# Kernel tuning notes

Measured on AMD Instinct MI355X. Metric: run time of the kernel, lower is better.

The kernel has to match this reference:

```python
import jax, jax.numpy as jnp
import numpy as np

B, N, D = 1, 128, 64
H, DH = 8, 64            # heads, per-head dim; dim_inner = dim*dim_head = 512
DI = H * DH              # 512
L = 2                    # max_degree
S = 1 + 2 * L            # 5 degree slots: (h, r_1..L, x_1..L)
MLP = 1024               # int(2.0 * dim_inner)
EPS = 1e-5


def _ln(x, g):
    m = x.mean(-1, keepdims=True)
    v = ((x - m) ** 2).mean(-1, keepdims=True)
    return (x - m) * jax.lax.rsqrt(v + EPS) * g


def setup_inputs() -> dict:
    key = jax.random.key(0)
    ks = jax.random.split(key, 16)
    rn = lambda k, s, sc=1.0: jax.random.normal(k, s, dtype=jnp.float32) * sc
    return {
        "h": rn(ks[0], (B, N, D)),
        "t_ij": rn(ks[1], (B, N, N, D)),
        "r1": rn(ks[2], (B, N, N, 3)),
        "r2": rn(ks[3], (B, N, N, 5)),
        "x1": rn(ks[4], (B, N, D, 3)),
        "x2": rn(ks[5], (B, N, D, 5)),
        "g_hi": jnp.ones((D,), jnp.float32),
        "g_hj": jnp.ones((D,), jnp.float32),
        "Wq": rn(ks[6], (D, DI), D ** -0.5),
        "Wk": rn(ks[7], (D, DI), D ** -0.5),
        "Wv1": rn(ks[8], (D, MLP), D ** -0.5),
        "bv1": jnp.zeros((MLP,), jnp.float32),
        "Wv2": rn(ks[9], (MLP, S * DI), MLP ** -0.5),
        "bv2": jnp.zeros((S * DI,), jnp.float32),
        "Wp1": rn(ks[10], (D, MLP), D ** -0.5),
        "bp1": jnp.zeros((MLP,), jnp.float32),
        "Wp2": rn(ks[11], (MLP, S * DI), MLP ** -0.5),
        "bp2": jnp.zeros((S * DI,), jnp.float32),
        "Wev": rn(ks[12], (D, S * DI), D ** -0.5),
        "Wc": rn(ks[13], (DI, D), DI ** -0.5),
    }


def reference(h, t_ij, r1, r2, x1, x2, g_hi, g_hj, Wq, Wk, Wv1, bv1, Wv2, bv2,
              Wp1, bp1, Wp2, bp2, Wev, Wc):
    b, n, d = h.shape
    hi, hj = _ln(h, g_hi), _ln(h, g_hj)
    q = (hi @ Wq).reshape(b, n, H, DH).transpose(0, 2, 1, 3)                # b h i d
    k = (hj @ Wk).reshape(b, n, H, DH).transpose(0, 2, 1, 3)                # b h j d
    vals = (jax.nn.silu(hj @ Wv1 + bv1) @ Wv2 + bv2)
    vals = vals.reshape(b, n, S, H, DH).transpose(0, 3, 1, 2, 4)            # b h j s d
    pav = (jax.nn.silu(hj @ Wp1 + bp1) @ Wp2 + bp2)
    pav = pav.reshape(b, n, S, H, DH).transpose(0, 3, 1, 2, 4)              # b h j s d
    # NOTE: source uses to_edge_values for BOTH edge keys and edge values (to_edge_keys is dead code)
    ev = (t_ij @ Wev).reshape(b, n, n, S, H, DH).transpose(0, 4, 1, 2, 3, 5)  # b h i j s d
    sim_num = jnp.einsum('bhid,bhjd->bhij', q, k)                           # b h i j
    sim_den = jnp.einsum('bhid,bhijsd->bhis', q, ev)                        # b h i s
    attn = sim_num[..., None] / sim_den[:, :, :, None, :]                   # b h i j s (quotient attention)
    sea = attn[..., None] * vals[:, :, None] + ev * pav[:, :, None]         # b h i j s d
    out = sea.transpose(0, 2, 3, 4, 1, 5).reshape(b, n, n, S, DI) @ Wc      # b i j s D
    # split sizes (1, L, L) along the s axis: h scale, r_ij scales, x scales
    h_new = h + out[:, :, :, 0, :].sum(axis=2)                              # sum over neighbors j
    xs, rs = (x1, x2), (r1, r2)
    x_new = [jnp.einsum('bjdm,bijd->bidm', xs[l], out[:, :, :, 1 + L + l, :])
             + jnp.einsum('bijm,bijd->bidm', rs[l], out[:, :, :, 1 + l, :])
             for l in range(L)]
    return (h_new, x_new[0], x_new[1])
```

## Files before the change

kernel.cpp:

```cpp
#include <hip/hip_runtime.h>
#include <hip/hip_bf16.h>

typedef __hip_bfloat16 bf16;
typedef __attribute__((ext_vector_type(8))) short short8;
typedef __attribute__((ext_vector_type(4))) float f32x4;

#define NN 128
#define DD_ 64
#define HH_ 8
#define DH_ 64
#define DI_ 512
#define SS_ 5
#define MLPD 1024
#define SDI 2560
#define KS2 4
#define KCM 64

__device__ __forceinline__ float wave_sum64(float v) {
#pragma unroll
    for (int off = 32; off > 0; off >>= 1) v += __shfl_xor(v, off, 64);
    return v;
}

__device__ __forceinline__ unsigned short f2bf_u(float f) {
    unsigned u = __float_as_uint(f);
    u += 0x7FFF + ((u >> 16) & 1);
    return (unsigned short)(u >> 16);
}
__device__ __forceinline__ float bfu2f(unsigned short s) {
    return __uint_as_float(((unsigned)s) << 16);
}
__device__ __forceinline__ unsigned pk2(unsigned short a, unsigned short b) {
    return (unsigned)a | ((unsigned)b << 16);
}

__global__ __launch_bounds__(256) void k_front(
    const float* __restrict__ h, const float* __restrict__ ghi, const float* __restrict__ ghj,
    const float* __restrict__ Wq, const float* __restrict__ Wk,
    const float* __restrict__ Wv1, const float* __restrict__ bv1,
    const float* __restrict__ Wp1, const float* __restrict__ bp1,
    float* __restrict__ q, float* __restrict__ k,
    float* __restrict__ a1, float* __restrict__ p1) {
    int i = blockIdx.x, ch = blockIdx.y, t = threadIdx.x;
    int d = t & 63;
    __shared__ float hib[DD_], hjb[DD_];
    float x = h[i * DD_ + d];
    float s = wave_sum64(x);
    float s2 = wave_sum64(x * x);
    float m = s * (1.0f / DD_);
    float v = s2 * (1.0f / DD_) - m * m;
    float r = rsqrtf(v + 1e-5f);
    float xc = (x - m) * r;
    if (t < 64) { hib[d] = xc * ghi[d]; hjb[d] = xc * ghj[d]; }
    __syncthreads();
    {
        int c = ch * 128 + (t & 127);
        const float* W = (t < 128) ? Wq : Wk;
        const float* hb = (t < 128) ? hib : hjb;
        float a = 0.f;
#pragma unroll 8
        for (int dd = 0; dd < DD_; dd++) a += hb[dd] * W[dd * DI_ + c];
        float* dstqk = (t < 128) ? q : k;
        dstqk[i * DI_ + c] = a;
    }
    {
        int c = ch * 256 + t;
        float av = 0.f, ap = 0.f;
#pragma unroll 4
        for (int dd = 0; dd < DD_; dd++) {
            float hv = hjb[dd];
            av += hv * Wv1[dd * MLPD + c];
            ap += hv * Wp1[dd * MLPD + c];
        }
        float xv = av + bv1[c], xp = ap + bp1[c];
        a1[i * MLPD + c] = xv / (1.0f + expf(-xv));
        p1[i * MLPD + c] = xp / (1.0f + expf(-xp));
    }
}

__global__ __launch_bounds__(256) void k_mid(
    const float* __restrict__ a1, const float* __restrict__ p1,
    const float* __restrict__ Wv2, const float* __restrict__ Wp2,
    float* __restrict__ part,
    const float* __restrict__ tij, const float* __restrict__ Wev,
    const float* __restrict__ q, float* __restrict__ rsd,
    const float* __restrict__ k, float* __restrict__ sn) {
    __shared__ __align__(16) unsigned char smem[30720];
    int b = blockIdx.x, t = threadIdx.x;
    if (b < 320) {
        unsigned short (*Ahi)[40] = (unsigned short (*)[40])(smem);
        unsigned short (*Alo)[40] = (unsigned short (*)[40])(smem + 10240);
        unsigned short (*Bhi)[40] = (unsigned short (*)[40])(smem + 20480);
        unsigned short (*Blo)[40] = (unsigned short (*)[40])(smem + 25600);
        int ct = b % 80, ks = b / 80;
        int c0 = ct * 64;
        bool isp = c0 >= 2560;
        int c0l = c0 - (isp ? 2560 : 0);
        const float* __restrict__ src = isp ? p1 : a1;
        const float* __restrict__ W = isp ? Wp2 : Wv2;
        int kbase = ks * 256;
        int lane = t & 63, wv = t >> 6;
        int l15 = lane & 15, quad = lane >> 4;
        f32x4 acc[2][4];
#pragma unroll
        for (int mt = 0; mt < 2; mt++)
#pragma unroll
            for (int nt = 0; nt < 4; nt++) acc[mt][nt] = (f32x4){0.f, 0.f, 0.f, 0.f};
        int aj = t >> 1, ak = (t & 1) * 16;
        int bc = t & 63, bk = (t >> 6) * 8;
        for (int kc = 0; kc < 8; kc++) {
            int k0 = kbase + kc * 32;
            __syncthreads();
            {
                unsigned short h16[16], l16[16];
                const float* ap = &src[(size_t)aj * MLPD + k0 + ak];
#pragma unroll
                for (int e = 0; e < 16; e += 4) {
                    float4 v = *(const float4*)(ap + e);
                    float vv[4] = {v.x, v.y, v.z, v.w};
#pragma unroll
                    for (int z = 0; z < 4; z++) {
                        unsigned short hb = f2bf_u(vv[z]);
                        h16[e + z] = hb;
                        l16[e + z] = f2bf_u(vv[z] - bfu2f(hb));
                    }
                }
                *(uint4*)&Ahi[aj][ak] = make_uint4(pk2(h16[0], h16[1]), pk2(h16[2], h16[3]),
                                                   pk2(h16[4], h16[5]), pk2(h16[6], h16[7]));
                *(uint4*)&Ahi[aj][ak + 8] = make_uint4(pk2(h16[8], h16[9]), pk2(h16[10], h16[11]),
                                                       pk2(h16[12], h16[13]), pk2(h16[14], h16[15]));
                *(uint4*)&Alo[aj][ak] = make_uint4(pk2(l16[0], l16[1]), pk2(l16[2], l16[3]),
                                                   pk2(l16[4], l16[5]), pk2(l16[6], l16[7]));
                *(uint4*)&Alo[aj][ak + 8] = make_uint4(pk2(l16[8], l16[9]), pk2(l16[10], l16[11]),
                                                       pk2(l16[12], l16[13]), pk2(l16[14], l16[15]));
            }
            {
                unsigned short h8[8], l8[8];
#pragma unroll
                for (int e = 0; e < 8; e++) {
                    float v = W[(size_t)(k0 + bk + e) * SDI + c0l + bc];
                    unsigned short hb = f2bf_u(v);
                    h8[e] = hb;
                    l8[e] = f2bf_u(v - bfu2f(hb));
                }
                *(uint4*)&Bhi[bc][bk] = make_uint4(pk2(h8[0], h8[1]), pk2(h8[2], h8[3]),
                                                   pk2(h8[4], h8[5]), pk2(h8[6], h8[7]));
                *(uint4*)&Blo[bc][bk] = make_uint4(pk2(l8[0], l8[1]), pk2(l8[2], l8[3]),
                                                   pk2(l8[4], l8[5]), pk2(l8[6], l8[7]));
            }
            __syncthreads();
            int ko = quad * 8;
            short8 a_h0 = *(const short8*)&Ahi[(wv * 2 + 0) * 16 + l15][ko];
            short8 a_l0 = *(const short8*)&Alo[(wv * 2 + 0) * 16 + l15][ko];
            short8 a_h1 = *(const short8*)&Ahi[(wv * 2 + 1) * 16 + l15][ko];
            short8 a_l1 = *(const short8*)&Alo[(wv * 2 + 1) * 16 + l15][ko];
#pragma unroll
            for (int nt = 0; nt < 4; nt++) {
                short8 b_h = *(const short8*)&Bhi[nt * 16 + l15][ko];
                short8 b_l = *(const short8*)&Blo[nt * 16 + l15][ko];
                acc[0][nt] = __builtin_amdgcn_mfma_f32_16x16x32_bf16(a_h0, b_h, acc[0][nt], 0, 0, 0);
                acc[0][nt] = __builtin_amdgcn_mfma_f32_16x16x32_bf16(a_h0, b_l, acc[0][nt], 0, 0, 0);
                acc[0][nt] = __builtin_amdgcn_mfma_f32_16x16x32_bf16(a_l0, b_h, acc[0][nt], 0, 0, 0);
                acc[1][nt] = __builtin_amdgcn_mfma_f32_16x16x32_bf16(a_h1, b_h, acc[1][nt], 0, 0, 0);
                acc[1][nt] = __builtin_amdgcn_mfma_f32_16x16x32_bf16(a_h1, b_l, acc[1][nt], 0, 0, 0);
                acc[1][nt] = __builtin_amdgcn_mfma_f32_16x16x32_bf16(a_l1, b_h, acc[1][nt], 0, 0, 0);
            }
        }
#pragma unroll
        for (int mt = 0; mt < 2; mt++)
#pragma unroll
            for (int nt = 0; nt < 4; nt++)
#pragma unroll
                for (int r = 0; r < 4; r++) {
                    int j = (wv * 2 + mt) * 16 + quad * 4 + r;
                    int cc = c0 + nt * 16 + l15;
                    part[(size_t)ks * 655360 + (size_t)j * 5120 + cc] = acc[mt][nt][r];
                }
    } else if (b < 448) {
        float* red = (float*)smem;
        float* Tl = (float*)(smem + 1024);
        float* ql = (float*)(smem + 1280);
        int i = b - 320;
        int c = t & 63, jw = t >> 6;
        float s = 0.f;
        for (int j = jw; j < NN; j += 4) s += tij[(size_t)(i * NN + j) * DD_ + c];
        red[jw * 64 + c] = s;
        ql[t] = q[i * DI_ + t];
        ql[t + 256] = q[i * DI_ + t + 256];
        __syncthreads();
        if (t < 64) Tl[t] = red[t] + red[64 + t] + red[128 + t] + red[192 + t];
        __syncthreads();
#pragma unroll
        for (int kx = 0; kx < 10; kx++) {
            int u = kx * 256 + t;
            float ev = 0.f;
#pragma unroll 8
            for (int cc = 0; cc < DD_; cc++) ev += Tl[cc] * Wev[(size_t)cc * SDI + u];
            float den = wave_sum64(ev * ql[u & 511]);
            if ((t & 63) == 0) {
                int g = u >> 6;
                int ss = g >> 3, hh = g & 7;
                rsd[i * 40 + hh * SS_ + ss] = 1.0f / den;
            }
        }
    } else {
        float* qb = (float*)smem;
        int idx = b - 448;
        int i = idx & 127, yh = idx >> 7;
        if (t < 128) qb[t] = q[i * DI_ + yh * 128 + t];
        __syncthreads();
        int hh = yh * 2 + (t >> 7), j = t & 127;
        float a = 0.f;
        const float* kr = &k[(size_t)j * DI_ + hh * DH_];
        const float* qr = &qb[(t >> 7) * 64];
#pragma unroll 8
        for (int d = 0; d < DH_; d++) a += qr[d] * kr[d];
        sn[i * 1024 + hh * NN + j] = a;
    }
}

__global__ __launch_bounds__(256) void k_mid2(
    const float* __restrict__ part, const float* __restrict__ bv2,
    const float* __restrict__ bp2, const float* __restrict__ Wc,
    const float* __restrict__ Wev, float* __restrict__ VC, float* __restrict__ M) {
    __shared__ __align__(16) unsigned char smem[38912];
    int b = blockIdx.x, t = threadIdx.x;
    if (b < 640) {
        float* vlds = (float*)smem;
        int j = b & 127, s = b >> 7;
#pragma unroll
        for (int r = 0; r < 2; r++) {
            int tt = r * 256 + t;
            int e = s * 512 + tt;
            float sum = 0.f;
#pragma unroll
            for (int p = 0; p < KS2; p++) sum += part[(size_t)p * 655360 + (size_t)j * 5120 + e];
            vlds[tt] = sum + bv2[e];
        }
        __syncthreads();
#pragma unroll
        for (int r = 0; r < 2; r++) {
            int tt = r * 256 + t;
            int dd = tt & 63;
            int hbase = tt - dd;
            float acc = 0.f;
#pragma unroll 8
            for (int d2 = 0; d2 < DH_; d2++)
                acc += vlds[hbase + d2] * Wc[(size_t)(hbase + d2) * DD_ + dd];
            VC[(size_t)(j * SS_ + s) * DI_ + tt] = acc;
        }
    } else {
        int idx = b - 640;
        int j = idx & 127, s = idx >> 7;
        int lane = t & 63, w = t >> 6;
        float* P = (float*)smem;
        unsigned short (*Ahi)[72] = (unsigned short (*)[72])(smem + 2048);
        unsigned short (*Alo)[72] = (unsigned short (*)[72])(smem + 11264);
        unsigned short (*Bhi)[72] = (unsigned short (*)[72])(smem + 20480);
        unsigned short (*Blo)[72] = (unsigned short (*)[72])(smem + 29696);
        {
            int e = 2560 + s * 512 + t;
            float s0 = 0.f, s1 = 0.f;
#pragma unroll
            for (int p = 0; p < KS2; p++) {
                s0 += part[(size_t)p * 655360 + (size_t)j * 5120 + e];
                s1 += part[(size_t)p * 655360 + (size_t)j * 5120 + e + 256];
            }
            P[t] = s0 + bp2[s * 512 + t];
            P[t + 256] = s1 + bp2[s * 512 + t + 256];
        }
        f32x4 acc[4];
#pragma unroll
        for (int n = 0; n < 4; n++) acc[n] = (f32x4){0.f, 0.f, 0.f, 0.f};
        __syncthreads();
        for (int u0 = 0; u0 < DI_; u0 += KCM) {
            {
                int c = t >> 2, ug = (t & 3) * 16;
                const float* wevp = &Wev[(size_t)c * SDI + s * DI_ + u0 + ug];
                unsigned short ah[16], al[16];
#pragma unroll
                for (int e = 0; e < 16; e += 4) {
                    float4 wv = *(const float4*)(wevp + e);
                    float4 pv = *(const float4*)&P[u0 + ug + e];
                    float av[4] = {wv.x * pv.x, wv.y * pv.y, wv.z * pv.z, wv.w * pv.w};
#pragma unroll
                    for (int z = 0; z < 4; z++) {
                        unsigned short hh2 = f2bf_u(av[z]);
                        ah[e + z] = hh2;
                        al[e + z] = f2bf_u(av[z] - bfu2f(hh2));
                    }
                }
                *(uint4*)&Ahi[c][ug] = make_uint4(pk2(ah[0], ah[1]), pk2(ah[2], ah[3]),
                                                  pk2(ah[4], ah[5]), pk2(ah[6], ah[7]));
                *(uint4*)&Ahi[c][ug + 8] = make_uint4(pk2(ah[8], ah[9]), pk2(ah[10], ah[11]),
                                                      pk2(ah[12], ah[13]), pk2(ah[14], ah[15]));
                *(uint4*)&Alo[c][ug] = make_uint4(pk2(al[0], al[1]), pk2(al[2], al[3]),
                                                  pk2(al[4], al[5]), pk2(al[6], al[7]));
                *(uint4*)&Alo[c][ug + 8] = make_uint4(pk2(al[8], al[9]), pk2(al[10], al[11]),
                                                      pk2(al[12], al[13]), pk2(al[14], al[15]));
            }
            {
                int dd = t & 63, ub = (t >> 6) * 16;
                unsigned short bh[16], bl[16];
#pragma unroll
                for (int e = 0; e < 16; e++) {
                    float v = Wc[(size_t)(u0 + ub + e) * DD_ + dd];
                    unsigned short hh2 = f2bf_u(v);
                    bh[e] = hh2;
                    bl[e] = f2bf_u(v - bfu2f(hh2));
                }
                *(uint4*)&Bhi[dd][ub] = make_uint4(pk2(bh[0], bh[1]), pk2(bh[2], bh[3]),
                                                   pk2(bh[4], bh[5]), pk2(bh[6], bh[7]));
                *(uint4*)&Bhi[dd][ub + 8] = make_uint4(pk2(bh[8], bh[9]), pk2(bh[10], bh[11]),
                                                       pk2(bh[12], bh[13]), pk2(bh[14], bh[15]));
                *(uint4*)&Blo[dd][ub] = make_uint4(pk2(bl[0], bl[1]), pk2(bl[2], bl[3]),
                                                   pk2(bl[4], bl[5]), pk2(bl[6], bl[7]));
                *(uint4*)&Blo[dd][ub + 8] = make_uint4(pk2(bl[8], bl[9]), pk2(bl[10], bl[11]),
                                                       pk2(bl[12], bl[13]), pk2(bl[14], bl[15]));
            }
            __syncthreads();
#pragma unroll
            for (int kk = 0; kk < 2; kk++) {
                int ko = kk * 32 + (lane >> 4) * 8;
                short8 a_h = *(const short8*)&Ahi[w * 16 + (lane & 15)][ko];
                short8 a_l = *(const short8*)&Alo[w * 16 + (lane & 15)][ko];
#pragma unroll
                for (int n = 0; n < 4; n++) {
                    short8 b_h = *(const short8*)&Bhi[n * 16 + (lane & 15)][ko];
                    short8 b_l = *(const short8*)&Blo[n * 16 + (lane & 15)][ko];
                    acc[n] = __builtin_amdgcn_mfma_f32_16x16x32_bf16(a_h, b_h, acc[n], 0, 0, 0);
                    acc[n] = __builtin_amdgcn_mfma_f32_16x16x32_bf16(a_h, b_l, acc[n], 0, 0, 0);
                    acc[n] = __builtin_amdgcn_mfma_f32_16x16x32_bf16(a_l, b_h, acc[n], 0, 0, 0);
                }
            }
            __syncthreads();
        }
        float* Mp = &M[(size_t)(j * SS_ + s) * 4096];
#pragma unroll
        for (int n = 0; n < 4; n++)
#pragma unroll
            for (int r = 0; r < 4; r++) {
                int c = w * 16 + (lane >> 4) * 4 + r;
                int dd = n * 16 + (lane & 15);
                Mp[c * 64 + dd] = acc[n][r];
            }
    }
}

__global__ __launch_bounds__(256) void k_out(const float* __restrict__ M, const float* __restrict__ VC,
                                             const float* __restrict__ sn, const float* __restrict__ rsd,
                                             const float* __restrict__ tij, float* __restrict__ outb) {
    int j = blockIdx.x, s = blockIdx.y, t = threadIdx.x;
    int lane = t & 63, wv = t >> 6, l15 = lane & 15, quad = lane >> 4;
    __shared__ unsigned short Ahi[128][40], Alo[128][40];
    __shared__ unsigned short Bhi[64][40], Blo[64][40];
    f32x4 acc[2][4];
#pragma unroll
    for (int mt = 0; mt < 2; mt++)
#pragma unroll
        for (int nt = 0; nt < 4; nt++) acc[mt][nt] = (f32x4){0.f, 0.f, 0.f, 0.f};
    {
        int i = t >> 1, hg = (t & 1) * 4;
        unsigned short h4[4], l4[4];
#pragma unroll
        for (int e = 0; e < 4; e++) {
            int hh_ = hg + e;
            float v = sn[i * 1024 + hh_ * NN + j] * rsd[i * 40 + hh_ * SS_ + s];
            unsigned short hb = f2bf_u(v);
            h4[e] = hb;
            l4[e] = f2bf_u(v - bfu2f(hb));
        }
        *(uint2*)&Ahi[i][hg] = make_uint2(pk2(h4[0], h4[1]), pk2(h4[2], h4[3]));
        *(uint2*)&Alo[i][hg] = make_uint2(pk2(l4[0], l4[1]), pk2(l4[2], l4[3]));
#pragma unroll
        for (int r = 0; r < 2; r++) {
            int idx = t + r * 256;
            if (idx < 384) {
                int ii = idx / 3, g = idx % 3;
                *(uint4*)&Ahi[ii][8 + g * 8] = make_uint4(0, 0, 0, 0);
                *(uint4*)&Alo[ii][8 + g * 8] = make_uint4(0, 0, 0, 0);
            }
        }
        if (t < 64) {
            unsigned short h8[8], l8[8];
#pragma unroll
            for (int e = 0; e < 8; e++) {
                float v = VC[(size_t)(j * SS_ + s) * DI_ + e * 64 + t];
                unsigned short hb = f2bf_u(v);
                h8[e] = hb;
                l8[e] = f2bf_u(v - bfu2f(hb));
            }
            *(uint4*)&Bhi[t][0] = make_uint4(pk2(h8[0], h8[1]), pk2(h8[2], h8[3]),
                                             pk2(h8[4], h8[5]), pk2(h8[6], h8[7]));
            *(uint4*)&Blo[t][0] = make_uint4(pk2(l8[0], l8[1]), pk2(l8[2], l8[3]),
                                             pk2(l8[4], l8[5]), pk2(l8[6], l8[7]));
        } else {
            int idx = t - 64;
            int dd2 = idx / 3, g = idx % 3;
            *(uint4*)&Bhi[dd2][8 + g * 8] = make_uint4(0, 0, 0, 0);
            *(uint4*)&Blo[dd2][8 + g * 8] = make_uint4(0, 0, 0, 0);
        }
    }
    __syncthreads();
    {
        int ko = quad * 8;
        short8 a_h0 = *(const short8*)&Ahi[(wv * 2 + 0) * 16 + l15][ko];
        short8 a_l0 = *(const short8*)&Alo[(wv * 2 + 0) * 16 + l15][ko];
        short8 a_h1 = *(const short8*)&Ahi[(wv * 2 + 1) * 16 + l15][ko];
        short8 a_l1 = *(const short8*)&Alo[(wv * 2 + 1) * 16 + l15][ko];
#pragma unroll
        for (int nt = 0; nt < 4; nt++) {
            short8 b_h = *(const short8*)&Bhi[nt * 16 + l15][ko];
            short8 b_l = *(const short8*)&Blo[nt * 16 + l15][ko];
            acc[0][nt] = __builtin_amdgcn_mfma_f32_16x16x32_bf16(a_h0, b_h, acc[0][nt], 0, 0, 0);
            acc[0][nt] = __builtin_amdgcn_mfma_f32_16x16x32_bf16(a_h0, b_l, acc[0][nt], 0, 0, 0);
            acc[0][nt] = __builtin_amdgcn_mfma_f32_16x16x32_bf16(a_l0, b_h, acc[0][nt], 0, 0, 0);
            acc[1][nt] = __builtin_amdgcn_mfma_f32_16x16x32_bf16(a_h1, b_h, acc[1][nt], 0, 0, 0);
            acc[1][nt] = __builtin_amdgcn_mfma_f32_16x16x32_bf16(a_h1, b_l, acc[1][nt], 0, 0, 0);
            acc[1][nt] = __builtin_amdgcn_mfma_f32_16x16x32_bf16(a_l1, b_h, acc[1][nt], 0, 0, 0);
        }
    }
    for (int kc = 0; kc < 2; kc++) {
        __syncthreads();
        {
            int i = t >> 1, chalf = (t & 1) * 16;
            unsigned short h16[16], l16[16];
            const float* tp = &tij[(size_t)(i * NN + j) * DD_ + kc * 32 + chalf];
#pragma unroll
            for (int e = 0; e < 16; e += 4) {
                float4 v = *(const float4*)(tp + e);
                float vv[4] = {v.x, v.y, v.z, v.w};
#pragma unroll
                for (int z = 0; z < 4; z++) {
                    unsigned short hb = f2bf_u(vv[z]);
                    h16[e + z] = hb;
                    l16[e + z] = f2bf_u(vv[z] - bfu2f(hb));
                }
            }
            *(uint4*)&Ahi[i][chalf] = make_uint4(pk2(h16[0], h16[1]), pk2(h16[2], h16[3]),
                                                 pk2(h16[4], h16[5]), pk2(h16[6], h16[7]));
            *(uint4*)&Ahi[i][chalf + 8] = make_uint4(pk2(h16[8], h16[9]), pk2(h16[10], h16[11]),
                                                     pk2(h16[12], h16[13]), pk2(h16[14], h16[15]));
            *(uint4*)&Alo[i][chalf] = make_uint4(pk2(l16[0], l16[1]), pk2(l16[2], l16[3]),
                                                 pk2(l16[4], l16[5]), pk2(l16[6], l16[7]));
            *(uint4*)&Alo[i][chalf + 8] = make_uint4(pk2(l16[8], l16[9]), pk2(l16[10], l16[11]),
                                                     pk2(l16[12], l16[13]), pk2(l16[14], l16[15]));
        }
        {
            int dd2 = t & 63, cg = (t >> 6) * 8;
            unsigned short h8[8], l8[8];
#pragma unroll
            for (int e = 0; e < 8; e++) {
                float v = M[(size_t)(j * SS_ + s) * 4096 + (size_t)(kc * 32 + cg + e) * 64 + dd2];
                unsigned short hb = f2bf_u(v);
                h8[e] = hb;
                l8[e] = f2bf_u(v - bfu2f(hb));
            }
            *(uint4*)&Bhi[dd2][cg] = make_uint4(pk2(h8[0], h8[1]), pk2(h8[2], h8[3]),
                                                pk2(h8[4], h8[5]), pk2(h8[6], h8[7]));
            *(uint4*)&Blo[dd2][cg] = make_uint4(pk2(l8[0], l8[1]), pk2(l8[2], l8[3]),
                                                pk2(l8[4], l8[5]), pk2(l8[6], l8[7]));
        }
        __syncthreads();
        int ko = quad * 8;
        short8 a_h0 = *(const short8*)&Ahi[(wv * 2 + 0) * 16 + l15][ko];
        short8 a_l0 = *(const short8*)&Alo[(wv * 2 + 0) * 16 + l15][ko];
        short8 a_h1 = *(const short8*)&Ahi[(wv * 2 + 1) * 16 + l15][ko];
        short8 a_l1 = *(const short8*)&Alo[(wv * 2 + 1) * 16 + l15][ko];
#pragma unroll
        for (int nt = 0; nt < 4; nt++) {
            short8 b_h = *(const short8*)&Bhi[nt * 16 + l15][ko];
            short8 b_l = *(const short8*)&Blo[nt * 16 + l15][ko];
            acc[0][nt] = __builtin_amdgcn_mfma_f32_16x16x32_bf16(a_h0, b_h, acc[0][nt], 0, 0, 0);
            acc[0][nt] = __builtin_amdgcn_mfma_f32_16x16x32_bf16(a_h0, b_l, acc[0][nt], 0, 0, 0);
            acc[0][nt] = __builtin_amdgcn_mfma_f32_16x16x32_bf16(a_l0, b_h, acc[0][nt], 0, 0, 0);
            acc[1][nt] = __builtin_amdgcn_mfma_f32_16x16x32_bf16(a_h1, b_h, acc[1][nt], 0, 0, 0);
            acc[1][nt] = __builtin_amdgcn_mfma_f32_16x16x32_bf16(a_h1, b_l, acc[1][nt], 0, 0, 0);
            acc[1][nt] = __builtin_amdgcn_mfma_f32_16x16x32_bf16(a_l1, b_h, acc[1][nt], 0, 0, 0);
        }
    }
#pragma unroll
    for (int mt = 0; mt < 2; mt++)
#pragma unroll
        for (int nt = 0; nt < 4; nt++)
#pragma unroll
            for (int r = 0; r < 4; r++) {
                int i = (wv * 2 + mt) * 16 + quad * 4 + r;
                int dd = nt * 16 + l15;
                outb[((size_t)(i * NN + j) * SS_ + s) * 64 + dd] = acc[mt][nt][r];
            }
}

__global__ __launch_bounds__(640) void k_redF(const float* __restrict__ outb,
                                              const float* __restrict__ r1, const float* __restrict__ r2,
                                              const float* __restrict__ x1, const float* __restrict__ x2,
                                              const float* __restrict__ h, float* __restrict__ dst) {
    int i = blockIdx.x, t = threadIdx.x;
    int half = (t >= 320) ? 1 : 0;
    int tt = t - half * 320;
    int s = tt >> 6, dd = tt & 63;
    float am[5] = {0.f, 0.f, 0.f, 0.f, 0.f};
    int jbeg = half * 64;
    for (int jj = 0; jj < 64; jj++) {
        int j = jbeg + jj;
        float ov = outb[((size_t)(i * NN + j) * SS_ + s) * 64 + dd];
        if (s == 0) {
            am[0] += ov;
        } else if (s == 1) {
#pragma unroll
            for (int m = 0; m < 3; m++) am[m] += r1[(i * NN + j) * 3 + m] * ov;
        } else if (s == 2) {
#pragma unroll
            for (int m = 0; m < 5; m++) am[m] += r2[(i * NN + j) * 5 + m] * ov;
        } else if (s == 3) {
#pragma unroll
            for (int m = 0; m < 3; m++) am[m] += x1[(j * DD_ + dd) * 3 + m] * ov;
        } else {
#pragma unroll
            for (int m = 0; m < 5; m++) am[m] += x2[(j * DD_ + dd) * 5 + m] * ov;
        }
    }
    __shared__ float lds[2][5][64][5];
#pragma unroll
    for (int m = 0; m < 5; m++) lds[half][s][dd][m] = am[m];
    __syncthreads();
    if (half == 0) {
        if (s == 0) {
            float v = lds[0][0][dd][0] + lds[1][0][dd][0];
            dst[i * DD_ + dd] = h[i * DD_ + dd] + v;
        } else if (s == 1) {
#pragma unroll
            for (int m = 0; m < 3; m++) {
                float v = lds[0][1][dd][m] + lds[1][1][dd][m] + lds[0][3][dd][m] + lds[1][3][dd][m];
                dst[8192 + (i * DD_ + dd) * 3 + m] = v;
            }
        } else if (s == 2) {
#pragma unroll
            for (int m = 0; m < 5; m++) {
                float v = lds[0][2][dd][m] + lds[1][2][dd][m] + lds[0][4][dd][m] + lds[1][4][dd][m];
                dst[8192 + 24576 + (i * DD_ + dd) * 5 + m] = v;
            }
        }
    }
}

extern "C" void kernel_launch(void* const* d_in, const int* in_sizes, int n_in,
                              void* d_out, int out_size, void* d_ws, size_t ws_size,
                              hipStream_t stream) {
    const float* h_in = (const float*)d_in[0];
    const float* tij = (const float*)d_in[1];
    const float* r1 = (const float*)d_in[2];
    const float* r2 = (const float*)d_in[3];
    const float* x1 = (const float*)d_in[4];
    const float* x2 = (const float*)d_in[5];
    const float* ghi = (const float*)d_in[6];
    const float* ghj = (const float*)d_in[7];
    const float* Wq = (const float*)d_in[8];
    const float* Wk = (const float*)d_in[9];
    const float* Wv1 = (const float*)d_in[10];
    const float* bv1 = (const float*)d_in[11];
    const float* Wv2 = (const float*)d_in[12];
    const float* bv2 = (const float*)d_in[13];
    const float* Wp1 = (const float*)d_in[14];
    const float* bp1 = (const float*)d_in[15];
    const float* Wp2 = (const float*)d_in[16];
    const float* bp2 = (const float*)d_in[17];
    const float* Wev = (const float*)d_in[18];
    const float* Wc = (const float*)d_in[19];
    float* dst = (float*)d_out;

    float* w = (float*)d_ws;
    size_t off = 16;
    auto alloc = [&](size_t n) { float* p = w + off; off += n; return p; };
    float* q    = alloc(65536);
    float* k    = alloc(65536);
    float* a1   = alloc(131072);
    float* p1   = alloc(131072);
    float* VC   = alloc(327680);
    float* sn   = alloc(131072);
    float* rsd  = alloc(5120);
    float* M    = alloc(2621440);
    float* outb = alloc(5242880);
    float* part = alloc(2621440);

    k_front<<<dim3(128, 4), dim3(256), 0, stream>>>(h_in, ghi, ghj, Wq, Wk, Wv1, bv1, Wp1, bp1,
                                                    q, k, a1, p1);
    k_mid<<<dim3(960), dim3(256), 0, stream>>>(a1, p1, Wv2, Wp2, part, tij, Wev, q, rsd, k, sn);
    k_mid2<<<dim3(1280), dim3(256), 0, stream>>>(part, bv2, bp2, Wc, Wev, VC, M);
    k_out<<<dim3(128, 5), dim3(256), 0, stream>>>(M, VC, sn, rsd, tij, outb);
    k_redF<<<dim3(128), dim3(640), 0, stream>>>(outb, r1, r2, x1, x2, h_in, dst);
}
```

Measured before the change: 238.1 us.

## Move t_ij neighbor reduction into front kernel and split edge-denominator work across blocks

The sum of t_ij over neighbors j is moved out of k_mid into 128 extra blocks of k_front, which write a T buffer. In k_mid, the 128 blocks that each did 10 passes of the Wev projection become 640 blocks that each do 2 passes over one 512-column chunk. The aim is to shorten the critical path of those heavy blocks and overlap the t_ij read with the front MLP work. The cost is an extra buffer round trip and more block launches, and each chunk block still reloads its row of q.

```diff
diff --git a/kernel.cpp b/kernel.cpp
--- a/kernel.cpp
+++ b/kernel.cpp
@@ -39,9 +39,22 @@
     const float* __restrict__ Wq, const float* __restrict__ Wk,
     const float* __restrict__ Wv1, const float* __restrict__ bv1,
     const float* __restrict__ Wp1, const float* __restrict__ bp1,
+    const float* __restrict__ tij,
     float* __restrict__ q, float* __restrict__ k,
-    float* __restrict__ a1, float* __restrict__ p1) {
-    int i = blockIdx.x, ch = blockIdx.y, t = threadIdx.x;
+    float* __restrict__ a1, float* __restrict__ p1, float* __restrict__ T) {
+    int b = blockIdx.x, t = threadIdx.x;
+    if (b >= 512) {
+        int i = b - 512;
+        __shared__ float red[4][64];
+        int c = t & 63, jg = t >> 6;
+        float s = 0.f;
+        for (int j = jg; j < NN; j += 4) s += tij[(size_t)(i * NN + j) * DD_ + c];
+        red[jg][c] = s;
+        __syncthreads();
+        if (t < 64) T[i * 64 + t] = red[0][t] + red[1][t] + red[2][t] + red[3][t];
+        return;
+    }
+    int i = b & 127, ch = b >> 7;
     int d = t & 63;
     __shared__ float hib[DD_], hjb[DD_];
     float x = h[i * DD_ + d];
@@ -82,7 +95,7 @@
     const float* __restrict__ a1, const float* __restrict__ p1,
     const float* __restrict__ Wv2, const float* __restrict__ Wp2,
     float* __restrict__ part,
-    const float* __restrict__ tij, const float* __restrict__ Wev,
+    const float* __restrict__ T, const float* __restrict__ Wev,
     const float* __restrict__ q, float* __restrict__ rsd,
     const float* __restrict__ k, float* __restrict__ sn) {
     __shared__ __align__(16) unsigned char smem[30720];
@@ -176,23 +189,18 @@
                     int cc = c0 + nt * 16 + l15;
                     part[(size_t)ks * 655360 + (size_t)j * 5120 + cc] = acc[mt][nt][r];
                 }
-    } else if (b < 448) {
-        float* red = (float*)smem;
-        float* Tl = (float*)(smem + 1024);
-        float* ql = (float*)(smem + 1280);
-        int i = b - 320;
-        int c = t & 63, jw = t >> 6;
-        float s = 0.f;
-        for (int j = jw; j < NN; j += 4) s += tij[(size_t)(i * NN + j) * DD_ + c];
-        red[jw * 64 + c] = s;
+    } else if (b < 960) {
+        float* Tl = (float*)smem;
+        float* ql = (float*)(smem + 256);
+        int idx = b - 320;
+        int i = idx & 127, chunk = idx >> 7;
+        if (t < 64) Tl[t] = T[i * 64 + t];
         ql[t] = q[i * DI_ + t];
         ql[t + 256] = q[i * DI_ + t + 256];
         __syncthreads();
-        if (t < 64) Tl[t] = red[t] + red[64 + t] + red[128 + t] + red[192 + t];
-        __syncthreads();
-#pragma unroll
-        for (int kx = 0; kx < 10; kx++) {
-            int u = kx * 256 + t;
+#pragma unroll
+        for (int kx = 0; kx < 2; kx++) {
+            int u = chunk * 512 + kx * 256 + t;
             float ev = 0.f;
 #pragma unroll 8
             for (int cc = 0; cc < DD_; cc++) ev += Tl[cc] * Wev[(size_t)cc * SDI + u];
@@ -205,7 +213,7 @@
         }
     } else {
         float* qb = (float*)smem;
-        int idx = b - 448;
+        int idx = b - 960;
         int i = idx & 127, yh = idx >> 7;
         if (t < 128) qb[t] = q[i * DI_ + yh * 128 + t];
         __syncthreads();
@@ -582,10 +590,11 @@
     float* M    = alloc(2621440);
     float* outb = alloc(5242880);
     float* part = alloc(2621440);
-
-    k_front<<<dim3(128, 4), dim3(256), 0, stream>>>(h_in, ghi, ghj, Wq, Wk, Wv1, bv1, Wp1, bp1,
-                                                    q, k, a1, p1);
-    k_mid<<<dim3(960), dim3(256), 0, stream>>>(a1, p1, Wv2, Wp2, part, tij, Wev, q, rsd, k, sn);
+    float* T    = alloc(8192);
+
+    k_front<<<dim3(640), dim3(256), 0, stream>>>(h_in, ghi, ghj, Wq, Wk, Wv1, bv1, Wp1, bp1,
+                                                 tij, q, k, a1, p1, T);
+    k_mid<<<dim3(1472), dim3(256), 0, stream>>>(a1, p1, Wv2, Wp2, part, T, Wev, q, rsd, k, sn);
     k_mid2<<<dim3(1280), dim3(256), 0, stream>>>(part, bv2, bp2, Wc, Wev, VC, M);
     k_out<<<dim3(128, 5), dim3(256), 0, stream>>>(M, VC, sn, rsd, tij, outb);
     k_redF<<<dim3(128), dim3(640), 0, stream>>>(outb, r1, r2, x1, x2, h_in, dst);
```

Result: faster. 213.6 us (-10.3%).
